# Kernel optimization log

Hardware: AMD Instinct MI355X
Metric: run time of the kernel (lower is better)

## Reference

```python
import jax, jax.numpy as jnp
import numpy as np

N_NODES = 20000
N_EDGES = 320000
EMB = 256
K_DIFF = 3
BN_EPS = 1e-5


def conv1d(x, w, b, stride):
    # x: [N, Cin, L], w: [Cout, Cin, K]
    y = jax.lax.conv_general_dilated(x, w, window_strides=(stride,), padding='VALID',
                                     dimension_numbers=('NCH', 'OIH', 'NCH'))
    return y + b[None, :, None]


def batchnorm_train(x, gamma, beta):
    # training-mode BatchNorm1d over (N, L) per channel, biased variance
    m = jnp.mean(x, axis=(0, 2), keepdims=True)
    v = jnp.var(x, axis=(0, 2), keepdims=True)
    return (x - m) * jax.lax.rsqrt(v + BN_EPS) * gamma[None, :, None] + beta[None, :, None]


def dconv(X, W, b, row, col, norm_out, norm_in, n):
    # Diffusion convolution (pytorch_geometric_temporal DConv), K hops,
    # forward (out-degree) and backward (in-degree) random walks.
    def prop(x, norm):
        msg = norm[:, None] * x[row]                    # [E, F] gather
        return jax.ops.segment_sum(msg, col, num_segments=n)  # scatter-add to targets

    K = W.shape[1]
    Tx_0 = X
    Tx_1 = X
    H = X @ W[0, 0] + X @ W[1, 0]
    if K > 1:
        Tx_1_o = prop(X, norm_out)
        Tx_1_i = prop(X, norm_in)
        H = H + Tx_1_o @ W[0, 1] + Tx_1_i @ W[1, 1]
    for k in range(2, K):
        Tx_2_o = 2.0 * prop(Tx_1_o, norm_out) - Tx_0
        Tx_2_i = 2.0 * prop(Tx_1_i, norm_in) - Tx_0
        H = H + Tx_2_o @ W[0, k] + Tx_2_i @ W[1, k]
        Tx_0, Tx_1_o, Tx_1_i = Tx_1, Tx_2_o, Tx_2_i
    return H + b


def setup_inputs() -> dict:
    key = jax.random.key(0)
    ks = jax.random.split(key, 16)
    d_in = 2 * EMB  # concat([X, H])
    inp = {
        'x': jax.random.normal(ks[0], (N_NODES, 1, 100), dtype=jnp.float32),
        'edge_index': jax.random.randint(ks[1], (2, N_EDGES), 0, N_NODES, dtype=jnp.int32),
        'hidden_state': jax.random.normal(ks[2], (N_NODES, EMB), dtype=jnp.float32),
        'conv1_w': jax.random.normal(ks[3], (32, 1, 10), dtype=jnp.float32) * 0.2,
        'conv1_b': jnp.zeros((32,), jnp.float32),
        'bn1_gamma': jnp.ones((32,), jnp.float32),
        'bn1_beta': jnp.zeros((32,), jnp.float32),
        'conv2_w': jax.random.normal(ks[4], (32, 32, 10), dtype=jnp.float32) * 0.05,
        'conv2_b': jnp.zeros((32,), jnp.float32),
        'bn2_gamma': jnp.ones((32,), jnp.float32),
        'bn2_beta': jnp.zeros((32,), jnp.float32),
        'W_z': jax.random.normal(ks[5], (2, K_DIFF, d_in, EMB), dtype=jnp.float32) * 0.05,
        'b_z': jnp.zeros((EMB,), jnp.float32),
        'W_r': jax.random.normal(ks[6], (2, K_DIFF, d_in, EMB), dtype=jnp.float32) * 0.05,
        'b_r': jnp.zeros((EMB,), jnp.float32),
        'W_h': jax.random.normal(ks[7], (2, K_DIFF, d_in, EMB), dtype=jnp.float32) * 0.05,
        'b_h': jnp.zeros((EMB,), jnp.float32),
    }
    return inp


def reference(x, edge_index, hidden_state, conv1_w, conv1_b, bn1_gamma, bn1_beta,
              conv2_w, conv2_b, bn2_gamma, bn2_beta, W_z, b_z, W_r, b_r, W_h, b_h):
    n = x.shape[0]
    # CNN embedding: conv -> relu -> bn, twice
    h = batchnorm_train(jax.nn.relu(conv1d(x, conv1_w, conv1_b, 3)), bn1_gamma, bn1_beta)
    h = batchnorm_train(jax.nn.relu(conv1d(h, conv2_w, conv2_b, 3)), bn2_gamma, bn2_beta)
    X = h.reshape(n, -1)  # [N, EMB]

    row, col = edge_index[0], edge_index[1]
    ones = jnp.ones((row.shape[0],), X.dtype)
    deg_out = jax.ops.segment_sum(ones, row, num_segments=n)
    deg_in = jax.ops.segment_sum(ones, col, num_segments=n)
    norm_out = (1.0 / deg_out)[row]
    norm_in = (1.0 / deg_in)[col]

    H0 = hidden_state
    XH = jnp.concatenate([X, H0], axis=1)
    Z = jax.nn.sigmoid(dconv(XH, W_z, b_z, row, col, norm_out, norm_in, n))
    R = jax.nn.sigmoid(dconv(XH, W_r, b_r, row, col, norm_out, norm_in, n))
    XRH = jnp.concatenate([X, R * H0], axis=1)
    H_tilde = jnp.tanh(dconv(XRH, W_h, b_h, row, col, norm_out, norm_in, n))
    H = Z * H0 + (1.0 - Z) * H_tilde
    return jax.nn.relu(H)
```

## Files before the change

### kernel.cpp

```cpp
#include <hip/hip_runtime.h>
#include <cstdint>
#include <cstddef>

#define NN 20000
#define NE 320000
#define SBUF 10240000

typedef float f32x4 __attribute__((ext_vector_type(4)));
typedef short s16x8 __attribute__((ext_vector_type(8)));
typedef unsigned short us;

__device__ __forceinline__ us f2bf(float x){
    unsigned u = __float_as_uint(x);
    unsigned r = (u + 0x7fffu + ((u >> 16) & 1u)) >> 16;
    return (us)r;
}
__device__ __forceinline__ float bf2f(us s){
    return __uint_as_float(((unsigned)s) << 16);
}

__device__ __forceinline__ void gl16(const void* g, void* l){
    __builtin_amdgcn_global_load_lds((const __attribute__((address_space(1))) unsigned int*)g,
                                     (__attribute__((address_space(3))) unsigned int*)l, 16, 0, 0);
}

__device__ __forceinline__ void upd8(uint4 v, float w, float* ao, float* ai){
    float f0=__uint_as_float(v.x<<16), f1=__uint_as_float(v.x&0xffff0000u);
    float f2=__uint_as_float(v.y<<16), f3=__uint_as_float(v.y&0xffff0000u);
    float f4=__uint_as_float(v.z<<16), f5=__uint_as_float(v.z&0xffff0000u);
    float f6=__uint_as_float(v.w<<16), f7=__uint_as_float(v.w&0xffff0000u);
    ao[0]=fmaf(w,f0,ao[0]); ao[1]=fmaf(w,f1,ao[1]); ao[2]=fmaf(w,f2,ao[2]); ao[3]=fmaf(w,f3,ao[3]);
    ao[4]=fmaf(w,f4,ao[4]); ao[5]=fmaf(w,f5,ao[5]); ao[6]=fmaf(w,f6,ao[6]); ao[7]=fmaf(w,f7,ao[7]);
    ai[0]+=f0; ai[1]+=f1; ai[2]+=f2; ai[3]+=f3; ai[4]+=f4; ai[5]+=f5; ai[6]+=f6; ai[7]+=f7;
}
__device__ __forceinline__ void updw(uint4 v, float w, float* a){
    float f0=__uint_as_float(v.x<<16), f1=__uint_as_float(v.x&0xffff0000u);
    float f2=__uint_as_float(v.y<<16), f3=__uint_as_float(v.y&0xffff0000u);
    float f4=__uint_as_float(v.z<<16), f5=__uint_as_float(v.z&0xffff0000u);
    float f6=__uint_as_float(v.w<<16), f7=__uint_as_float(v.w&0xffff0000u);
    a[0]=fmaf(w,f0,a[0]); a[1]=fmaf(w,f1,a[1]); a[2]=fmaf(w,f2,a[2]); a[3]=fmaf(w,f3,a[3]);
    a[4]=fmaf(w,f4,a[4]); a[5]=fmaf(w,f5,a[5]); a[6]=fmaf(w,f6,a[6]); a[7]=fmaf(w,f7,a[7]);
}
__device__ __forceinline__ uint4 pack8(const float* a){
    uint4 r;
    r.x=((unsigned)f2bf(a[1])<<16)|f2bf(a[0]);
    r.y=((unsigned)f2bf(a[3])<<16)|f2bf(a[2]);
    r.z=((unsigned)f2bf(a[5])<<16)|f2bf(a[4]);
    r.w=((unsigned)f2bf(a[7])<<16)|f2bf(a[6]);
    return r;
}
__device__ __forceinline__ uint4 pack8s(const float* a, float s){
    uint4 r;
    r.x=((unsigned)f2bf(s*a[1])<<16)|f2bf(s*a[0]);
    r.y=((unsigned)f2bf(s*a[3])<<16)|f2bf(s*a[2]);
    r.z=((unsigned)f2bf(s*a[5])<<16)|f2bf(s*a[4]);
    r.w=((unsigned)f2bf(s*a[7])<<16)|f2bf(s*a[6]);
    return r;
}


__global__ void k_zero(uint32_t* p, int n){
    int i = blockIdx.x*256 + threadIdx.x;
    if(i < n) p[i] = 0u;
}

__global__ void k_degree(const int* __restrict__ ei, int* degout, int* degin){
    int e = blockIdx.x*256 + threadIdx.x;
    if(e < NE){
        atomicAdd(&degout[ei[e]], 1);
        atomicAdd(&degin[ei[NE+e]], 1);
    }
}

__global__ void k_scan(const int* __restrict__ degin, int* __restrict__ coloff,
                       float* __restrict__ invdegin){
    __shared__ int part[1024];
    int t = threadIdx.x;
    int base = t*20;
    int s = 0;
    for(int k=0;k<20;k++){ int i = base+k; if(i < NN) s += degin[i]; }
    part[t] = s;
    __syncthreads();
    for(int off=1; off<1024; off<<=1){
        int v = (t>=off) ? part[t-off] : 0;
        __syncthreads();
        part[t] += v;
        __syncthreads();
    }
    int run = (t>0) ? part[t-1] : 0;
    for(int k=0;k<20;k++){
        int i = base+k;
        if(i < NN){
            int d = degin[i];
            coloff[i] = run;
            run += d;
            invdegin[i] = (d>0) ? (1.0f/(float)d) : 0.0f;
        }
    }
    if(t==1023) coloff[NN] = part[1023];
}

__global__ void k_csr(const int* __restrict__ ei, const int* __restrict__ degout,
                      const int* __restrict__ coloff, int* cnt, int2* __restrict__ ew){
    int e = blockIdx.x*256 + threadIdx.x;
    if(e < NE){
        int r = ei[e], c = ei[NE+e];
        int pos = coloff[c] + atomicAdd(&cnt[c], 1);
        int2 v; v.x = r; v.y = __float_as_int(1.0f/(float)degout[r]);
        ew[pos] = v;
    }
}


__global__ void k_conv1(const float* __restrict__ x, const float* __restrict__ w1,
                        const float* __restrict__ b1, us* __restrict__ y1T){
    __shared__ float w[320];
    __shared__ float bb[32];
    int t = threadIdx.x;
    for(int i=t;i<320;i+=256) w[i] = w1[i];
    if(t < 32) bb[t] = b1[t];
    __syncthreads();
    int gid = blockIdx.x*256 + t;
    int node = gid>>5, p = gid&31;
    us* yo = y1T + (size_t)node*1024 + p*32;
    if(p >= 31){
        uint4 z = {0,0,0,0};
        *(uint4*)yo = z; *(uint4*)(yo+8) = z;
        *(uint4*)(yo+16) = z; *(uint4*)(yo+24) = z;
        return;
    }
    const float* xr = x + node*100 + 3*p;
    float xv[10];
    #pragma unroll
    for(int k=0;k<10;k++) xv[k] = xr[k];
    float o[32];
    #pragma unroll
    for(int c=0;c<32;c++){
        float a = bb[c];
        #pragma unroll
        for(int k=0;k<10;k++) a = fmaf(w[c*10+k], xv[k], a);
        o[c] = fmaxf(a, 0.0f);
    }
    *(uint4*)yo      = pack8(o);
    *(uint4*)(yo+8)  = pack8(o+8);
    *(uint4*)(yo+16) = pack8(o+16);
    *(uint4*)(yo+24) = pack8(o+24);
}

__global__ void k_chanstats_T(const us* __restrict__ y, float* __restrict__ sq){
    int tid = blockIdx.x*256 + threadIdx.x;
    int slot = tid & 1023;
    int c = slot & 31;
    int node0 = tid >> 10;
    float s = 0.f, q = 0.f;
    for(int n=node0; n<NN; n+=64){
        float v = bf2f(y[(size_t)n*1024 + slot]);
        s += v; q = fmaf(v, v, q);
    }
    s += __shfl_xor(s, 32);
    q += __shfl_xor(q, 32);
    if((threadIdx.x & 63) < 32){
        atomicAdd(&sq[c], s);
        atomicAdd(&sq[32+c], q);
    }
}

template<int SLOTS, int PPC>
__global__ void k_chanstats_bf(const us* __restrict__ y, float* __restrict__ sq){
    int tid = blockIdx.x*blockDim.x + threadIdx.x;
    int slot = tid & (SLOTS-1);
    int node0 = tid / SLOTS;
    int nstride = (gridDim.x*blockDim.x) / SLOTS;
    int c = slot / PPC;
    float s = 0.f, q = 0.f;
    for(int n=node0; n<NN; n+=nstride){
        float v = bf2f(y[(size_t)n*SLOTS + slot]);
        s += v; q = fmaf(v, v, q);
    }
    #pragma unroll
    for(int m=PPC>>1; m>0; m>>=1){
        s += __shfl_xor(s, m);
        q += __shfl_xor(q, m);
    }
    if((threadIdx.x & (PPC-1)) == 0){
        atomicAdd(&sq[c], s);
        atomicAdd(&sq[32+c], q);
    }
}

__global__ void k_bnfin(const float* __restrict__ sq, const float* __restrict__ gamma,
                        const float* __restrict__ beta, float* __restrict__ scsh,
                        float inv_count){
    int c = threadIdx.x;
    if(c < 32){
        float m = sq[c]*inv_count;
        float v = sq[32+c]*inv_count - m*m;
        float sc = gamma[c]*rsqrtf(v + 1e-5f);
        scsh[c] = sc;
        scsh[32+c] = beta[c] - m*sc;
    }
}

__global__ void k_wfold(const float* __restrict__ w2, const float* __restrict__ scsh1,
                        us* __restrict__ Bf){
    int idx = blockIdx.x*256 + threadIdx.x;
    if(idx >= 10240) return;
    int kk = idx >> 10, c2 = (idx >> 5) & 31, c = idx & 31;
    Bf[idx] = f2bf(scsh1[c] * w2[c2*320 + c*10 + kk]);
}

__global__ void k_wbias(const float* __restrict__ w2, const float* __restrict__ scsh1,
                        const float* __restrict__ b2, float* __restrict__ biasc){
    int t = threadIdx.x;
    int c2 = t >> 3, part = t & 7;
    float s = 0.f;
    for(int i=part; i<320; i+=8)
        s += scsh1[32 + i/10] * w2[c2*320 + i];
    s += __shfl_xor(s,1); s += __shfl_xor(s,2); s += __shfl_xor(s,4);
    if(part == 0) biasc[c2] = b2[c2] + s;
}

__global__ void __launch_bounds__(256) k_conv2m(const us* __restrict__ y1T,
        const us* __restrict__ Bf, const float* __restrict__ biasc,
        us* __restrict__ Xpre){
    int t = threadIdx.x;
    int wv = t>>6, l = t&63;
    int l15 = l&15, g = l>>4;
    int r0 = blockIdx.x*64 + wv*16;
    int arow = r0 + l15;
    int an = arow>>3, ap = arow&7;
    const us* abase = y1T + (size_t)an*1024 + (3*ap)*32 + g*8;
    const us* bbase = Bf + (size_t)l15*32 + g*8;
    f32x4 acc0 = {}, acc1 = {};
    #pragma unroll
    for(int kk=0;kk<10;kk++){
        s16x8 af = *(const s16x8*)(abase + kk*32);
        s16x8 b0 = *(const s16x8*)(bbase + kk*1024);
        s16x8 b1 = *(const s16x8*)(bbase + kk*1024 + 512);
        acc0 = __builtin_amdgcn_mfma_f32_16x16x32_bf16(af, b0, acc0, 0, 0, 0);
        acc1 = __builtin_amdgcn_mfma_f32_16x16x32_bf16(af, b1, acc1, 0, 0, 0);
    }
    int base = r0 + g*4;
    int n = base>>3, p0 = base&7;
    #pragma unroll
    for(int nf=0;nf<2;nf++){
        int c2 = nf*16 + l15;
        float bb = biasc[c2];
        f32x4 a = nf ? acc1 : acc0;
        float v0 = fmaxf(a[0]+bb,0.f), v1 = fmaxf(a[1]+bb,0.f);
        float v2 = fmaxf(a[2]+bb,0.f), v3 = fmaxf(a[3]+bb,0.f);
        uint2 pk;
        pk.x = ((unsigned)f2bf(v1)<<16)|f2bf(v0);
        pk.y = ((unsigned)f2bf(v3)<<16)|f2bf(v2);
        *(uint2*)&Xpre[(size_t)n*256 + c2*8 + p0] = pk;
    }
}

__global__ void __launch_bounds__(256) k_prep(const us* __restrict__ Xpre,
        const float* __restrict__ scsh, const float* __restrict__ h0,
        us* __restrict__ XHp){
    int node = blockIdx.x*4 + (threadIdx.x>>6);
    if(node >= NN) return;
    int lane = threadIdx.x & 63;
    int half = lane>>5, g = lane&31;
    uint4 o;
    if(half == 0){
        uint4 v = *(const uint4*)(Xpre + (size_t)node*256 + g*8);
        float sc = scsh[g], sh = scsh[32+g];
        float y[8];
        y[0]=fmaf(sc,__uint_as_float(v.x<<16),sh); y[1]=fmaf(sc,__uint_as_float(v.x&0xffff0000u),sh);
        y[2]=fmaf(sc,__uint_as_float(v.y<<16),sh); y[3]=fmaf(sc,__uint_as_float(v.y&0xffff0000u),sh);
        y[4]=fmaf(sc,__uint_as_float(v.z<<16),sh); y[5]=fmaf(sc,__uint_as_float(v.z&0xffff0000u),sh);
        y[6]=fmaf(sc,__uint_as_float(v.w<<16),sh); y[7]=fmaf(sc,__uint_as_float(v.w&0xffff0000u),sh);
        o = pack8(y);
    }else{
        float4 a = *(const float4*)(h0 + (size_t)node*256 + g*8);
        float4 b = *(const float4*)(h0 + (size_t)node*256 + g*8 + 4);
        float y[8] = {a.x,a.y,a.z,a.w,b.x,b.y,b.z,b.w};
        o = pack8(y);
    }
    *(uint4*)(XHp + (size_t)node*512 + (size_t)g*16 + half*8) = o;
}


__device__ __forceinline__ float weff_val(const float* W, int term, size_t base){
    const size_t S = 512*256;
    if(term==0)      return W[0*S+base] + W[3*S+base] - W[2*S+base] - W[5*S+base];
    else if(term==1) return W[1*S+base];
    else if(term==2) return W[4*S+base];
    else if(term==3) return 2.0f*W[2*S+base];
    else             return 2.0f*W[5*S+base];
}

template<int NCOL>
__global__ void __launch_bounds__(256) k_wefft(const float* __restrict__ Wa,
        const float* __restrict__ Wb, us* __restrict__ Wt){
    __shared__ float tile[64*65];
    int bx = blockIdx.x;
    constexpr int CT = NCOL/64;
    int kb = bx / (CT*4);
    int rem = bx % (CT*4);
    int ct = rem >> 2, rt = rem & 3;
    int col0 = ct*64, rr0 = rt*64;
    const float* W = (col0 < 256) ? Wa : Wb;
    int jb = col0 & 255;
    int term = kb >> 1, half = kb & 1;
    int t = threadIdx.x;
    int j_l = t & 63, r4 = t >> 6;
    #pragma unroll
    for(int it=0; it<16; it++){
        int rr_l = it*4 + r4;
        int row = half*256 + rr0 + rr_l;
        size_t base = (size_t)row*256 + jb + j_l;
        tile[j_l*65 + rr_l] = weff_val(W, term, base);
    }
    __syncthreads();
    int rr_w = t & 63;
    #pragma unroll
    for(int it=0; it<16; it++){
        int col_l = it*4 + r4;
        Wt[(size_t)(col0+col_l)*2560 + kb*256 + rr0 + rr_w] = f2bf(tile[col_l*65 + rr_w]);
    }
}


__global__ void __launch_bounds__(256) k_prop1(const us* __restrict__ XHp,
        const int* __restrict__ coloff, const int2* __restrict__ ew,
        const float* __restrict__ invdeg, us* __restrict__ T1op, us* __restrict__ T1ip){
    int node = blockIdx.x*4 + (threadIdx.x>>6);
    if(node >= NN) return;
    int lane = threadIdx.x & 63;
    size_t lo = (size_t)(lane&31)*16 + (lane>>5)*8;
    int s = __builtin_amdgcn_readfirstlane(coloff[node]);
    int e = __builtin_amdgcn_readfirstlane(coloff[node+1]);
    float ao[8]={0,0,0,0,0,0,0,0}, ai[8]={0,0,0,0,0,0,0,0};
    int j = s;
    for(; j+7 < e; j += 8){
        int2 ed[8]; uint4 v[8];
        #pragma unroll
        for(int i=0;i<8;i++) ed[i] = ew[j+i];
        #pragma unroll
        for(int i=0;i<8;i++) v[i] = *(const uint4*)(XHp+(size_t)ed[i].x*512+lo);
        #pragma unroll
        for(int i=0;i<8;i++) upd8(v[i], __int_as_float(ed[i].y), ao, ai);
    }
    for(; j < e; j++){
        int2 ed = ew[j];
        uint4 v = *(const uint4*)(XHp+(size_t)ed.x*512+lo);
        upd8(v, __int_as_float(ed.y), ao, ai);
    }
    float wi = invdeg[node];
    *(uint4*)(T1op+(size_t)node*512+lo) = pack8(ao);
    *(uint4*)(T1ip+(size_t)node*512+lo) = pack8s(ai,wi);
}

__global__ void __launch_bounds__(256) k_prop2(const us* __restrict__ T1op,
        const us* __restrict__ T1ip,
        const int* __restrict__ coloff, const int2* __restrict__ ew,
        const float* __restrict__ invdeg, us* __restrict__ P2op, us* __restrict__ P2ip){
    int node = blockIdx.x*4 + (threadIdx.x>>6);
    if(node >= NN) return;
    int lane = threadIdx.x & 63;
    size_t lo = (size_t)(lane&31)*16 + (lane>>5)*8;
    int s = __builtin_amdgcn_readfirstlane(coloff[node]);
    int e = __builtin_amdgcn_readfirstlane(coloff[node+1]);
    float ao[8]={0,0,0,0,0,0,0,0}, ai[8]={0,0,0,0,0,0,0,0};
    int j = s;
    for(; j+3 < e; j += 4){
        int2 ed[4]; uint4 va[4], vb[4];
        #pragma unroll
        for(int i=0;i<4;i++) ed[i] = ew[j+i];
        #pragma unroll
        for(int i=0;i<4;i++){
            size_t o = (size_t)ed[i].x*512+lo;
            va[i] = *(const uint4*)(T1op+o);
            vb[i] = *(const uint4*)(T1ip+o);
        }
        #pragma unroll
        for(int i=0;i<4;i++){
            updw(va[i], __int_as_float(ed[i].y), ao);
            updw(vb[i], 1.0f, ai);
        }
    }
    for(; j < e; j++){
        int2 ed = ew[j];
        size_t o = (size_t)ed.x*512+lo;
        updw(*(const uint4*)(T1op+o), __int_as_float(ed.y), ao);
        updw(*(const uint4*)(T1ip+o), 1.0f, ai);
    }
    float wi = invdeg[node];
    *(uint4*)(P2op+(size_t)node*512+lo) = pack8(ao);
    *(uint4*)(P2ip+(size_t)node*512+lo) = pack8s(ai,wi);
}

__global__ void __launch_bounds__(256) k_propq1(const us* __restrict__ RHb,
        const int* __restrict__ coloff, const int2* __restrict__ ew,
        const float* __restrict__ invdeg, us* __restrict__ Q1p){
    int node = blockIdx.x*4 + (threadIdx.x>>6);
    if(node >= NN) return;
    int lane = threadIdx.x & 63;
    int half = lane>>5, g = lane&31;
    int s = __builtin_amdgcn_readfirstlane(coloff[node]);
    int e = __builtin_amdgcn_readfirstlane(coloff[node+1]);
    float ao[8]={0,0,0,0,0,0,0,0}, ai[8]={0,0,0,0,0,0,0,0};
    int j = s;
    for(; j+3 < e; j += 4){
        int2 e0 = ew[j+half], e1 = ew[j+2+half];
        uint4 v0 = *(const uint4*)(RHb+(size_t)e0.x*256+g*8);
        uint4 v1 = *(const uint4*)(RHb+(size_t)e1.x*256+g*8);
        upd8(v0, __int_as_float(e0.y), ao, ai);
        upd8(v1, __int_as_float(e1.y), ao, ai);
    }
    for(; j+1 < e; j += 2){
        int2 ed = ew[j+half];
        uint4 v = *(const uint4*)(RHb+(size_t)ed.x*256+g*8);
        upd8(v, __int_as_float(ed.y), ao, ai);
    }
    if(j < e && half == 0){
        int2 ed = ew[j];
        uint4 v = *(const uint4*)(RHb+(size_t)ed.x*256+g*8);
        upd8(v, __int_as_float(ed.y), ao, ai);
    }
    #pragma unroll
    for(int k=0;k<8;k++){
        ao[k] += __shfl_xor(ao[k],32);
        ai[k] += __shfl_xor(ai[k],32);
    }
    if(half == 0){
        float wi = invdeg[node];
        *(uint4*)(Q1p+(size_t)node*512+(size_t)g*16)   = pack8(ao);
        *(uint4*)(Q1p+(size_t)node*512+(size_t)g*16+8) = pack8s(ai,wi);
    }
}

__global__ void __launch_bounds__(256) k_propu(const us* __restrict__ Yin,
        const int* __restrict__ coloff, const int2* __restrict__ ew,
        const float* __restrict__ invdeg, us* __restrict__ Pout){
    int node = blockIdx.x*4 + (threadIdx.x>>6);
    if(node >= NN) return;
    int lane = threadIdx.x & 63;
    int half = lane>>5;
    size_t lo = (size_t)(lane&31)*16 + half*8;
    int s = __builtin_amdgcn_readfirstlane(coloff[node]);
    int e = __builtin_amdgcn_readfirstlane(coloff[node+1]);
    float a[8]={0,0,0,0,0,0,0,0};
    int j = s;
    for(; j+7 < e; j += 8){
        int2 ed[8]; uint4 v[8];
        #pragma unroll
        for(int i=0;i<8;i++) ed[i] = ew[j+i];
        #pragma unroll
        for(int i=0;i<8;i++) v[i] = *(const uint4*)(Yin+(size_t)ed[i].x*512+lo);
        #pragma unroll
        for(int i=0;i<8;i++) updw(v[i], half ? 1.0f : __int_as_float(ed[i].y), a);
    }
    for(; j < e; j++){
        int2 ed = ew[j];
        uint4 v = *(const uint4*)(Yin+(size_t)ed.x*512+lo);
        updw(v, half ? 1.0f : __int_as_float(ed.y), a);
    }
    float sc = half ? invdeg[node] : 1.0f;
    *(uint4*)(Pout+(size_t)node*512+lo) = pack8s(a,sc);
}


template<int MODE, int BNT>
__global__ void __launch_bounds__(256) k_gemm(const us* __restrict__ XG,
        const us* __restrict__ RG, const us* __restrict__ Wt,
        const float* __restrict__ bias0, const float* __restrict__ bias1,
        const float* __restrict__ h0, const float* __restrict__ Zin,
        float* __restrict__ out0, us* __restrict__ out1){
    constexpr int WN = BNT/32;
    constexpr int NB = BNT/64;
    constexpr int NVM = 1 + NB;
    __shared__ us As[2][2048];
    __shared__ us Bs[2][BNT*32];
    int t = threadIdx.x;
    int wid = t >> 6, lane = t & 63;
    int l15 = lane & 15, kg = lane >> 4;

    int bid = blockIdx.x;
    int xcd = bid & 7, sblk = bid >> 3;
    int cidx = sblk & 3, r = (sblk >> 2)*8 + xcd;
    if(r >= 313) return;
    int row0 = r*64, col0 = cidx*BNT;
    int rowbase = (wid >> 1)*32, colbase = (wid & 1)*(BNT/2);
    int swz = (l15 >> 1) & 3;

    int srA = t >> 2;
    int sgA = (t & 3) ^ ((srA >> 1) & 3);
    int grA = row0 + srA; grA = (grA < NN) ? grA : NN-1;
    size_t rowoffA = (size_t)grA*512 + (size_t)sgA*16;
    int srB[NB], sgB[NB];
    size_t coloffB[NB];
    #pragma unroll
    for(int i=0;i<NB;i++){
        int c = t + i*256;
        srB[i] = c >> 2;
        sgB[i] = (c & 3) ^ ((srB[i] >> 1) & 3);
        coloffB[i] = (size_t)(col0+srB[i])*2560 + (size_t)sgB[i]*8;
    }

    f32x4 acc[2][WN] = {};

    auto stage = [&](int buf, int s){
        int kb = s >> 3;
        int ktc = (s & 7) * 4;
        if(MODE == 1 && kb == 1){
            gl16(RG + (rowoffA >> 1) + (size_t)ktc*8, &As[buf][t*8]);
        }else{
            const us* Ap;
            if(MODE == 0){
                Ap = XG + (size_t)(kb >> 1) * SBUF + (size_t)(kb & 1) * 8;
            }else{
                if((kb & 1) == 0) Ap = XG + (size_t)(kb >> 1) * SBUF;
                else Ap = RG + (size_t)((kb + 1) >> 2) * SBUF + (size_t)(((kb + 1) >> 1) & 1) * 8;
            }
            gl16(Ap + rowoffA + (size_t)ktc*16, &As[buf][t*8]);
        }
        const us* Wp = Wt + (size_t)kb*256 + (s & 7)*32;
        #pragma unroll
        for(int i=0;i<NB;i++)
            gl16(Wp + coloffB[i], &Bs[buf][(t+i*256)*8]);
    };

    stage(0, 0);
    stage(1, 1);
    for(int step=0; step<80; ++step){
        int cur = step & 1;
        if(step < 79){
            if(NVM == 3) asm volatile("s_waitcnt vmcnt(3)" ::: "memory");
            else         asm volatile("s_waitcnt vmcnt(2)" ::: "memory");
        }else{
            asm volatile("s_waitcnt vmcnt(0)" ::: "memory");
        }
        __builtin_amdgcn_s_barrier();
        s16x8 af[2], bfr[WN];
        #pragma unroll
        for(int i=0;i<2;i++){
            int row = rowbase + i*16 + l15;
            af[i] = *(const s16x8*)&As[cur][(row*4 + (kg ^ swz))*8];
        }
        #pragma unroll
        for(int n=0;n<WN;n++){
            int colr = colbase + n*16 + l15;
            bfr[n] = *(const s16x8*)&Bs[cur][(colr*4 + (kg ^ swz))*8];
        }
        asm volatile("s_waitcnt lgkmcnt(0)" ::: "memory");
        __builtin_amdgcn_sched_barrier(0);
        __builtin_amdgcn_s_barrier();
        if(step < 78) stage(cur, step+2);
        __builtin_amdgcn_s_setprio(1);
        #pragma unroll
        for(int mi=0;mi<2;mi++){
            #pragma unroll
            for(int ni=0;ni<WN;ni++){
                acc[mi][ni] = __builtin_amdgcn_mfma_f32_16x16x32_bf16(
                    af[mi], bfr[ni], acc[mi][ni], 0, 0, 0);
            }
        }
        __builtin_amdgcn_s_setprio(0);
    }

    #pragma unroll
    for(int mi=0;mi<2;mi++){
        int gr0 = row0 + rowbase + mi*16 + kg*4;
        #pragma unroll
        for(int ni=0;ni<WN;ni++){
            int j = col0 + colbase + ni*16 + l15;
            #pragma unroll
            for(int rr=0;rr<4;rr++){
                int gr = gr0 + rr;
                if(gr < NN){
                    float a = acc[mi][ni][rr];
                    if(MODE == 0){
                        if(j < 256){
                            out0[(size_t)gr*256 + j] = 1.0f/(1.0f + expf(-(a + bias0[j])));
                        }else{
                            int jj = j - 256;
                            float rv = 1.0f/(1.0f + expf(-(a + bias1[jj])));
                            out1[(size_t)gr*256 + jj] = f2bf(rv * h0[(size_t)gr*256 + jj]);
                        }
                    }else{
                        float z = Zin[(size_t)gr*256 + j];
                        float ht = tanhf(a + bias0[j]);
                        float H = z*h0[(size_t)gr*256 + j] + (1.0f - z)*ht;
                        out0[(size_t)gr*256 + j] = fmaxf(H, 0.0f);
                    }
                }
            }
        }
    }
}


extern "C" void kernel_launch(void* const* d_in, const int* in_sizes, int n_in,
                              void* d_out, int out_size, void* d_ws, size_t ws_size,
                              hipStream_t stream){
    const float* x   = (const float*)d_in[0];
    const int*   ei  = (const int*)  d_in[1];
    const float* h0  = (const float*)d_in[2];
    const float* w1  = (const float*)d_in[3];
    const float* b1  = (const float*)d_in[4];
    const float* g1  = (const float*)d_in[5];
    const float* be1 = (const float*)d_in[6];
    const float* w2  = (const float*)d_in[7];
    const float* b2  = (const float*)d_in[8];
    const float* g2  = (const float*)d_in[9];
    const float* be2 = (const float*)d_in[10];
    const float* Wz  = (const float*)d_in[11];
    const float* bz  = (const float*)d_in[12];
    const float* Wr  = (const float*)d_in[13];
    const float* br  = (const float*)d_in[14];
    const float* Wh  = (const float*)d_in[15];
    const float* bh  = (const float*)d_in[16];
    float* out = (float*)d_out;
    float* wsf = (float*)d_ws;
    (void)in_sizes; (void)n_in; (void)out_size;

    const size_t O_DEGO=0, O_DEGI=20000, O_CNT=40000, O_BN=60000;
    const size_t O_COLOFF=60288, O_EW=80384, O_INVDEG=720384;
    const size_t O_WTZR=740480, O_WTH=1395840;
    const size_t O_XPRE=1723520;
    const size_t O_XG=4283520;
    const size_t O_RG=29883520;
    const size_t O_Z=45243520;
    const size_t O_BF=50363520;
    const size_t WS_NEED_BYTES = (size_t)50366080 * 4;
    if(ws_size < WS_NEED_BYTES) return;

    const size_t SW = 5120000;

    int* degout = (int*)(wsf + O_DEGO);
    int* degin  = (int*)(wsf + O_DEGI);
    int* cnt    = (int*)(wsf + O_CNT);
    float* bn   = wsf + O_BN;
    int* coloff = (int*)(wsf + O_COLOFF);
    int2* ew    = (int2*)(wsf + O_EW);
    float* invdeg = wsf + O_INVDEG;
    us* Wtzr = (us*)(wsf + O_WTZR);
    us* Wth  = (us*)(wsf + O_WTH);
    us* Xpre = (us*)(wsf + O_XPRE);
    us* XG   = (us*)(wsf + O_XG);
    us* RG   = (us*)(wsf + O_RG);
    us* XHp  = XG;
    us* T1op = (us*)(wsf + O_XG + SW);
    us* T1ip = (us*)(wsf + O_XG + 2*SW);
    us* P2op = (us*)(wsf + O_XG + 3*SW);
    us* P2ip = (us*)(wsf + O_XG + 4*SW);
    us* RHb  = RG;
    us* Q1p  = (us*)(wsf + O_RG + SW);
    us* Q2p  = (us*)(wsf + O_RG + 2*SW);
    float* Z = wsf + O_Z;
    us* Bf   = (us*)(wsf + O_BF);
    us* y1T  = T1op;

    k_zero<<<236,256,0,stream>>>((uint32_t*)(wsf + O_DEGO), 60256);
    k_degree<<<1250,256,0,stream>>>(ei, degout, degin);
    k_scan<<<1,1024,0,stream>>>(degin, coloff, invdeg);
    k_csr<<<1250,256,0,stream>>>(ei, degout, coloff, cnt, ew);

    k_conv1<<<2500,256,0,stream>>>(x, w1, b1, y1T);
    k_chanstats_T<<<256,256,0,stream>>>(y1T, bn+0);
    k_bnfin<<<1,32,0,stream>>>(bn+0, g1, be1, bn+64, 1.0f/620000.0f);
    k_wfold<<<40,256,0,stream>>>(w2, bn+64, Bf);
    k_wbias<<<1,256,0,stream>>>(w2, bn+64, b2, bn+256);
    k_conv2m<<<2500,256,0,stream>>>(y1T, Bf, bn+256, Xpre);
    k_chanstats_bf<256,8><<<64,256,0,stream>>>(Xpre, bn+128);
    k_bnfin<<<1,32,0,stream>>>(bn+128, g2, be2, bn+192, 1.0f/160000.0f);
    k_prep<<<5000,256,0,stream>>>(Xpre, bn+192, h0, XHp);

    k_wefft<512><<<320,256,0,stream>>>(Wz, Wr, Wtzr);
    k_wefft<256><<<160,256,0,stream>>>(Wh, Wh, Wth);

    k_prop1<<<5000,256,0,stream>>>(XHp, coloff, ew, invdeg, T1op, T1ip);
    k_prop2<<<5000,256,0,stream>>>(T1op, T1ip, coloff, ew, invdeg, P2op, P2ip);

    k_gemm<0,128><<<1280,256,0,stream>>>(XG, RG, Wtzr, bz, br, h0, nullptr, Z, RHb);

    k_propq1<<<5000,256,0,stream>>>(RHb, coloff, ew, invdeg, Q1p);
    k_propu<<<5000,256,0,stream>>>(Q1p, coloff, ew, invdeg, Q2p);

    k_gemm<1,64><<<1280,256,0,stream>>>(XG, RG, Wth, bh, nullptr, h0, Z, out, nullptr);
}
```

Before: 720.1 us.

## Enlarge GEMM row tile to 128 and merge weight-fold kernels

The two GEMM kernels now compute 128-row tiles instead of 64, with each wave holding four row fragments. This halves the block count and increases reuse of each loaded weight tile, at the cost of more LDS, more accumulator registers, and fewer blocks for latency hiding. The vmcnt waits are adjusted to the extra A loads. Separately, the weight-fold and bias kernels are merged into one launch to save a kernel dispatch.

```diff
diff --git a/kernel.cpp b/kernel.cpp
--- a/kernel.cpp
+++ b/kernel.cpp
@@ -201,23 +201,23 @@
     }
 }
 
-__global__ void k_wfold(const float* __restrict__ w2, const float* __restrict__ scsh1,
-                        us* __restrict__ Bf){
-    int idx = blockIdx.x*256 + threadIdx.x;
-    if(idx >= 10240) return;
-    int kk = idx >> 10, c2 = (idx >> 5) & 31, c = idx & 31;
-    Bf[idx] = f2bf(scsh1[c] * w2[c2*320 + c*10 + kk]);
-}
-
-__global__ void k_wbias(const float* __restrict__ w2, const float* __restrict__ scsh1,
-                        const float* __restrict__ b2, float* __restrict__ biasc){
+__global__ void k_wprep(const float* __restrict__ w2, const float* __restrict__ scsh1,
+                        const float* __restrict__ b2, us* __restrict__ Bf,
+                        float* __restrict__ biasc){
+    int b = blockIdx.x;
     int t = threadIdx.x;
-    int c2 = t >> 3, part = t & 7;
-    float s = 0.f;
-    for(int i=part; i<320; i+=8)
-        s += scsh1[32 + i/10] * w2[c2*320 + i];
-    s += __shfl_xor(s,1); s += __shfl_xor(s,2); s += __shfl_xor(s,4);
-    if(part == 0) biasc[c2] = b2[c2] + s;
+    if(b < 40){
+        int idx = b*256 + t;
+        int kk = idx >> 10, c2 = (idx >> 5) & 31, c = idx & 31;
+        Bf[idx] = f2bf(scsh1[c] * w2[c2*320 + c*10 + kk]);
+    }else{
+        int c2 = t >> 3, part = t & 7;
+        float s = 0.f;
+        for(int i=part; i<320; i+=8)
+            s += scsh1[32 + i/10] * w2[c2*320 + i];
+        s += __shfl_xor(s,1); s += __shfl_xor(s,2); s += __shfl_xor(s,4);
+        if(part == 0) biasc[c2] = b2[c2] + s;
+    }
 }
 
 __global__ void __launch_bounds__(256) k_conv2m(const us* __restrict__ y1T,
@@ -472,8 +472,7 @@
         float* __restrict__ out0, us* __restrict__ out1){
     constexpr int WN = BNT/32;
     constexpr int NB = BNT/64;
-    constexpr int NVM = 1 + NB;
-    __shared__ us As[2][2048];
+    __shared__ us As[2][4096];
     __shared__ us Bs[2][BNT*32];
     int t = threadIdx.x;
     int wid = t >> 6, lane = t & 63;
@@ -482,15 +481,22 @@
     int bid = blockIdx.x;
     int xcd = bid & 7, sblk = bid >> 3;
     int cidx = sblk & 3, r = (sblk >> 2)*8 + xcd;
-    if(r >= 313) return;
-    int row0 = r*64, col0 = cidx*BNT;
-    int rowbase = (wid >> 1)*32, colbase = (wid & 1)*(BNT/2);
+    if(r >= 157) return;
+    int row0 = r*128, col0 = cidx*BNT;
+    int rowbase = (wid >> 1)*64, colbase = (wid & 1)*(BNT/2);
     int swz = (l15 >> 1) & 3;
 
-    int srA = t >> 2;
-    int sgA = (t & 3) ^ ((srA >> 1) & 3);
-    int grA = row0 + srA; grA = (grA < NN) ? grA : NN-1;
-    size_t rowoffA = (size_t)grA*512 + (size_t)sgA*16;
+    int srA[2], sgA[2];
+    size_t rowoffA[2];
+    #pragma unroll
+    for(int i=0;i<2;i++){
+        int c = t + i*256;
+        srA[i] = c >> 2;
+        sgA[i] = (c & 3) ^ ((srA[i] >> 1) & 3);
+        int gr = row0 + srA[i];
+        gr = (gr < NN) ? gr : NN-1;
+        rowoffA[i] = (size_t)gr*512 + (size_t)sgA[i]*16;
+    }
     int srB[NB], sgB[NB];
     size_t coloffB[NB];
     #pragma unroll
@@ -501,13 +507,15 @@
         coloffB[i] = (size_t)(col0+srB[i])*2560 + (size_t)sgB[i]*8;
     }
 
-    f32x4 acc[2][WN] = {};
+    f32x4 acc[4][WN] = {};
 
     auto stage = [&](int buf, int s){
         int kb = s >> 3;
         int ktc = (s & 7) * 4;
         if(MODE == 1 && kb == 1){
-            gl16(RG + (rowoffA >> 1) + (size_t)ktc*8, &As[buf][t*8]);
+            #pragma unroll
+            for(int i=0;i<2;i++)
+                gl16(RG + (rowoffA[i] >> 1) + (size_t)ktc*8, &As[buf][(t+i*256)*8]);
         }else{
             const us* Ap;
             if(MODE == 0){
@@ -516,7 +524,9 @@
                 if((kb & 1) == 0) Ap = XG + (size_t)(kb >> 1) * SBUF;
                 else Ap = RG + (size_t)((kb + 1) >> 2) * SBUF + (size_t)(((kb + 1) >> 1) & 1) * 8;
             }
-            gl16(Ap + rowoffA + (size_t)ktc*16, &As[buf][t*8]);
+            #pragma unroll
+            for(int i=0;i<2;i++)
+                gl16(Ap + rowoffA[i] + (size_t)ktc*16, &As[buf][(t+i*256)*8]);
         }
         const us* Wp = Wt + (size_t)kb*256 + (s & 7)*32;
         #pragma unroll
@@ -529,15 +539,15 @@
     for(int step=0; step<80; ++step){
         int cur = step & 1;
         if(step < 79){
-            if(NVM == 3) asm volatile("s_waitcnt vmcnt(3)" ::: "memory");
-            else         asm volatile("s_waitcnt vmcnt(2)" ::: "memory");
+            if(MODE == 0) asm volatile("s_waitcnt vmcnt(4)" ::: "memory");
+            else          asm volatile("s_waitcnt vmcnt(3)" ::: "memory");
         }else{
             asm volatile("s_waitcnt vmcnt(0)" ::: "memory");
         }
         __builtin_amdgcn_s_barrier();
-        s16x8 af[2], bfr[WN];
-        #pragma unroll
-        for(int i=0;i<2;i++){
+        s16x8 af[4], bfr[WN];
+        #pragma unroll
+        for(int i=0;i<4;i++){
             int row = rowbase + i*16 + l15;
             af[i] = *(const s16x8*)&As[cur][(row*4 + (kg ^ swz))*8];
         }
@@ -552,7 +562,7 @@
         if(step < 78) stage(cur, step+2);
         __builtin_amdgcn_s_setprio(1);
         #pragma unroll
-        for(int mi=0;mi<2;mi++){
+        for(int mi=0;mi<4;mi++){
             #pragma unroll
             for(int ni=0;ni<WN;ni++){
                 acc[mi][ni] = __builtin_amdgcn_mfma_f32_16x16x32_bf16(
@@ -563,7 +573,7 @@
     }
 
     #pragma unroll
-    for(int mi=0;mi<2;mi++){
+    for(int mi=0;mi<4;mi++){
         int gr0 = row0 + rowbase + mi*16 + kg*4;
         #pragma unroll
         for(int ni=0;ni<WN;ni++){
@@ -663,8 +673,7 @@
     k_conv1<<<2500,256,0,stream>>>(x, w1, b1, y1T);
     k_chanstats_T<<<256,256,0,stream>>>(y1T, bn+0);
     k_bnfin<<<1,32,0,stream>>>(bn+0, g1, be1, bn+64, 1.0f/620000.0f);
-    k_wfold<<<40,256,0,stream>>>(w2, bn+64, Bf);
-    k_wbias<<<1,256,0,stream>>>(w2, bn+64, b2, bn+256);
+    k_wprep<<<41,256,0,stream>>>(w2, bn+64, b2, Bf, bn+256);
     k_conv2m<<<2500,256,0,stream>>>(y1T, Bf, bn+256, Xpre);
     k_chanstats_bf<256,8><<<64,256,0,stream>>>(Xpre, bn+128);
     k_bnfin<<<1,32,0,stream>>>(bn+128, g2, be2, bn+192, 1.0f/160000.0f);
@@ -676,10 +685,10 @@
     k_prop1<<<5000,256,0,stream>>>(XHp, coloff, ew, invdeg, T1op, T1ip);
     k_prop2<<<5000,256,0,stream>>>(T1op, T1ip, coloff, ew, invdeg, P2op, P2ip);
 
-    k_gemm<0,128><<<1280,256,0,stream>>>(XG, RG, Wtzr, bz, br, h0, nullptr, Z, RHb);
+    k_gemm<0,128><<<640,256,0,stream>>>(XG, RG, Wtzr, bz, br, h0, nullptr, Z, RHb);
 
     k_propq1<<<5000,256,0,stream>>>(RHb, coloff, ew, invdeg, Q1p);
     k_propu<<<5000,256,0,stream>>>(Q1p, coloff, ew, invdeg, Q2p);
 
-    k_gemm<1,64><<<1280,256,0,stream>>>(XG, RG, Wth, bh, nullptr, h0, Z, out, nullptr);
-}
+    k_gemm<1,64><<<640,256,0,stream>>>(XG, RG, Wth, bh, nullptr, h0, Z, out, nullptr);
+}
```

Result: no change. 707.0 us, median of 2 (-1.8%).
